# Kernel tuning notes

Hardware: AMD Instinct MI355X
Metric: run time of the kernel (lower is better)

## Reference

```python
import jax, jax.numpy as jnp
import numpy as np

HID, XD, ZD, K = 512, 128, 64, 3
B, T = 64, 1024

def setup_inputs() -> dict:
    key = jax.random.key(0)
    ks = jax.random.split(key, 10)
    s = lambda *d: 1.0 / np.sqrt(d[0])
    return {
        "x_seq": jax.random.normal(ks[0], (B, T, XD), jnp.float32),
        "conv_w": jax.random.normal(ks[1], (K, XD, HID), jnp.float32) * (1.0/np.sqrt(K*XD)),
        "conv_b": jnp.zeros((HID,), jnp.float32),
        "Wx": jax.random.normal(ks[2], (HID, 4*HID), jnp.float32) * (1.0/np.sqrt(HID)),
        "Wh": jax.random.normal(ks[3], (HID, 4*HID), jnp.float32) * (1.0/np.sqrt(HID)),
        "b": jnp.zeros((4*HID,), jnp.float32),
        "W1": jax.random.normal(ks[4], (HID, HID), jnp.float32) * (1.0/np.sqrt(HID)),
        "b1": jnp.zeros((HID,), jnp.float32),
        "W2": jax.random.normal(ks[5], (HID, 2*ZD), jnp.float32) * (1.0/np.sqrt(HID)),
        "b2": jnp.zeros((2*ZD,), jnp.float32),
    }

def _forward(x_seq, conv_w, conv_b, Wx, Wh, b, W1, b1, W2, b2):
    # Conv1D, SAME padding: (B, T, x_dim) -> (B, T, HID)
    conv = jax.lax.conv_general_dilated(
        x_seq, conv_w, window_strides=(1,), padding="SAME",
        dimension_numbers=("NWC", "WIO", "NWC")) + conv_b

    def step(carry, x_t):
        c, h = carry
        # flax LSTMCell: gates i,f,g,o; input dense (no bias) + hidden dense (bias)
        z = x_t @ Wx + h @ Wh + b  # (B, 4*HID)
        i, f, g, o = jnp.split(z, 4, axis=-1)
        i, f, o = jax.nn.sigmoid(i), jax.nn.sigmoid(f), jax.nn.sigmoid(o)
        g = jnp.tanh(g)
        c_new = f * c + i * g
        h_new = o * jnp.tanh(c_new)
        return (c_new, h_new), h_new

    c0 = jnp.zeros((conv.shape[0], HID), conv.dtype)
    h0 = jnp.zeros((conv.shape[0], HID), conv.dtype)
    _, h_seq = jax.lax.scan(step, (c0, h0), jnp.swapaxes(conv, 0, 1))  # (T, B, HID)
    h_seq = jnp.swapaxes(h_seq, 0, 1)  # (B, T, HID)

    # per-step 2-layer MLP head, applied vectorized over (B, T)
    x = jax.nn.relu(h_seq @ W1 + b1)
    out = x @ W2 + b2  # (B, T, 2*ZD)
    mu, log_sigma = jnp.split(out, 2, axis=-1)
    return mu, log_sigma

def reference(x_seq, conv_w, conv_b, Wx, Wh, b, W1, b1, W2, b2):
    return _forward(x_seq, conv_w, conv_b, Wx, Wh, b, W1, b1, W2, b2)
```

## Files before the change

### kernel.cpp

```cpp
#include <hip/hip_runtime.h>
#include <math.h>

typedef unsigned short u16;
typedef unsigned int   u32;
typedef unsigned long long u64;
typedef _Float16 f16;
typedef __attribute__((ext_vector_type(8))) _Float16 f16x8;
typedef __attribute__((ext_vector_type(4))) float    f32x4;

#define T_SEQ 1024
#define NB    64
#define HID   512
#define KC    384
#define G4    2048
#define MR    (NB*T_SEQ)
#define ZD2   128

__device__ __align__(16) f16   g_xwin[(size_t)MR*KC];
__device__ __align__(16) f16   g_cwxt[(size_t)G4*KC];
__device__              float  g_bb[G4];
__device__ __align__(16) f16   g_whT[(size_t)G4*HID];
__device__ __align__(16) f16   g_w1T[(size_t)HID*HID];
__device__ __align__(16) f16   g_w2T[(size_t)ZD2*HID];
__device__              float  g_b1f[HID];
__device__              float  g_b2f[ZD2];
__device__ __align__(16) float g_XW[(size_t)MR*G4];
__device__ __align__(16) f16   g_hseq[(size_t)MR*HID];
__device__ __align__(16) f16   g_tmp1[(size_t)MR*HID];
__device__ __align__(16) u64   g_hstep[(size_t)(T_SEQ+1)*NB*128];
__device__              int    g_flags[T_SEQ*64];
__device__              int    g_in_fp32;

__device__ inline float bf2f(u16 u){ union{u32 i; float f;} v; v.i = ((u32)u)<<16; return v.f; }
__device__ inline u16  f2bf(float f){ union{u32 i; float f;} v; v.f = f; u32 u = v.i;
                                      return (u16)((u + 0x7fffu + ((u>>16)&1u))>>16); }
__device__ inline float load_in(const void* p, size_t i){
  return g_in_fp32 ? ((const float*)p)[i] : bf2f(((const u16*)p)[i]);
}
__device__ inline float fsig(float x){
  return __builtin_amdgcn_rcpf(1.f + __builtin_amdgcn_exp2f(-1.44269504f*x));
}
__device__ inline float ftanh(float x){
  x = fminf(fmaxf(x, -10.f), 10.f);
  float e = __builtin_amdgcn_exp2f(2.88539008f*x);
  return (e - 1.f) * __builtin_amdgcn_rcpf(e + 1.f);
}

__global__ void k_probe(const void* x){
  __shared__ int cnt;
  if (threadIdx.x == 0) cnt = 0;
  __syncthreads();
  int loc = 0;
  for (int i = threadIdx.x; i < 4096; i += 256){
    float a = fabsf(bf2f(((const u16*)x)[i]));
    if (a > 0.01f && a < 10.f) loc++;
  }
  atomicAdd(&cnt, loc);
  __syncthreads();
  if (threadIdx.x == 0) g_in_fp32 = (cnt < 3276) ? 1 : 0;
}

__global__ void k_init(const void* b1, const void* b2){
  int i = blockIdx.x*256 + threadIdx.x;
  if (i < HID)        g_b1f[i] = load_in(b1, i);
  if (i < ZD2)        g_b2f[i] = load_in(b2, i);
  if (i < T_SEQ*64)   g_flags[i] = 0;
  if (i < NB*128)     g_hstep[i] = 0ULL;
}

__global__ void k_combine(const void* conv_w, const void* conv_b, const void* Wx, const void* b){
  int j  = blockIdx.x*256 + threadIdx.x;
  int kc = blockIdx.y;
  float acc = 0.f;
  if (kc < KC){
    for (int m = 0; m < HID; ++m)
      acc += load_in(conv_w, (size_t)kc*HID + m) * load_in(Wx, (size_t)m*G4 + j);
    g_cwxt[(size_t)j*KC + kc] = (f16)acc;
  } else {
    for (int m = 0; m < HID; ++m)
      acc += load_in(conv_b, m) * load_in(Wx, (size_t)m*G4 + j);
    g_bb[j] = acc + load_in(b, j);
  }
}

__device__ inline void trans_body(const void* src, f16* dst, int R, int C){
  size_t i = (size_t)blockIdx.x*256 + threadIdx.x;
  if (i >= (size_t)R*C) return;
  int c = (int)(i / (size_t)R), r = (int)(i % (size_t)R);
  dst[i] = (f16)load_in(src, (size_t)r*C + c);
}
__global__ void k_trans_wh(const void* Wh){ trans_body(Wh, g_whT, HID, G4); }
__global__ void k_trans_w1(const void* W1){ trans_body(W1, g_w1T, HID, HID); }
__global__ void k_trans_w2(const void* W2){ trans_body(W2, g_w2T, HID, ZD2); }

__global__ void k_xwin(const void* x){
  size_t i = (size_t)blockIdx.x*256 + threadIdx.x;
  if (i >= (size_t)MR*KC) return;
  int row = (int)(i / KC), kc = (int)(i % KC);
  int k = kc >> 7, c = kc & 127;
  int b = row >> 10, t = row & 1023;
  int ts = t - 1 + k;
  float v = 0.f;
  if (ts >= 0 && ts < T_SEQ) v = load_in(x, ((size_t)b*T_SEQ + ts)*128 + c);
  g_xwin[i] = (f16)v;
}

template<int MODE, int K>
__device__ inline void gemm_body(const f16* __restrict__ A, const f16* __restrict__ BT,
                                 const float* __restrict__ bias, void* __restrict__ C, int N){
  const int tid = threadIdx.x;
  const int w = tid >> 6, lane = tid & 63;
  const int q = lane >> 4, ln = lane & 15;
  const int n0 = blockIdx.x * 128;
  const int m0 = blockIdx.y * 64;
  const f16* ap = A + (size_t)(m0 + w*16 + ln)*K + q*8;
  const f16* bp = BT + (size_t)(n0 + ln)*K + q*8;
  f32x4 acc[8] = {};
  #pragma unroll 4
  for (int k = 0; k < K; k += 32){
    f16x8 af = *(const f16x8*)(ap + k);
    #pragma unroll
    for (int nt = 0; nt < 8; ++nt){
      f16x8 bf = *(const f16x8*)(bp + (size_t)nt*16*K + k);
      acc[nt] = __builtin_amdgcn_mfma_f32_16x16x32_f16(af, bf, acc[nt], 0, 0, 0);
    }
  }
  const int f32o = g_in_fp32;
  #pragma unroll
  for (int nt = 0; nt < 8; ++nt){
    const int col = n0 + nt*16 + ln;
    const float bv = bias[col];
    #pragma unroll
    for (int r = 0; r < 4; ++r){
      const int row = m0 + w*16 + q*4 + r;
      float v = acc[nt][r] + bv;
      if (MODE == 0){
        ((float*)C)[(size_t)row*N + col] = v;
      } else if (MODE == 1){
        ((f16*)C)[(size_t)row*N + col] = (f16)fmaxf(v, 0.f);
      } else {
        size_t idx = (col < 64) ? ((size_t)row*64 + col)
                                : (4194304UL + (size_t)row*64 + (size_t)(col - 64));
        if (f32o) ((float*)C)[idx] = v;
        else      ((u16*)C)[idx]   = f2bf(v);
      }
    }
  }
}
__global__ __launch_bounds__(256) void k_gemm_xw(){   gemm_body<0,KC >(g_xwin, g_cwxt, g_bb,  g_XW,   G4 ); }
__global__ __launch_bounds__(256) void k_gemm_mlp1(){ gemm_body<1,HID>(g_hseq, g_w1T,  g_b1f, g_tmp1, HID); }
__global__ __launch_bounds__(256) void k_gemm_mlp2(void* out){ gemm_body<2,HID>(g_tmp1, g_w2T, g_b2f, out, ZD2); }

__global__ __launch_bounds__(256) void k_lstm(){
  __shared__ __align__(16) f16 whs[32*520];
  const int g   = blockIdx.x;
  const int tid = threadIdx.x;
  const int w = tid >> 6, lane = tid & 63;
  const int q = lane >> 4, ln = lane & 15;

  for (int idx = tid; idx < 32*HID; idx += 256){
    int r = idx >> 9, k = idx & 511;
    int zcol = (r >> 3)*HID + g*8 + (r & 7);
    whs[r*520 + k] = g_whT[(size_t)zcol*HID + k];
  }
  __syncthreads();

  const int  c8 = ln & 7;
  const bool lo = ln < 8;
  const int  zc0  = (lo ? 0 : HID)       + g*8 + c8;
  const int  zc1  = (lo ? 2*HID : 3*HID) + g*8 + c8;
  const int  colh = g*8 + c8;
  const int  am   = w*16 + ln;
  float c_st[4] = {0.f, 0.f, 0.f, 0.f};

  for (int t = 0; t < T_SEQ; ++t){
    float xwa[4], xwb[4];
    #pragma unroll
    for (int r = 0; r < 4; ++r){
      size_t base = ((size_t)((w*16 + q*4 + r)*T_SEQ + t))*G4;
      xwa[r] = g_XW[base + zc0];
      xwb[r] = g_XW[base + zc1];
    }
    if (t > 0){
      if (tid < 64){
        while (__hip_atomic_load(&g_flags[(t-1)*64 + tid],
                                 __ATOMIC_RELAXED, __HIP_MEMORY_SCOPE_AGENT) == 0) {}
      }
      __syncthreads();
    }
    const u64* hrow = g_hstep + ((size_t)t*NB + am)*128 + q*2;
    u64 hv[32];
    #pragma unroll
    for (int kk = 0; kk < 16; ++kk){
      hv[2*kk]   = __hip_atomic_load(hrow + (size_t)kk*8,     __ATOMIC_RELAXED, __HIP_MEMORY_SCOPE_AGENT);
      hv[2*kk+1] = __hip_atomic_load(hrow + (size_t)kk*8 + 1, __ATOMIC_RELAXED, __HIP_MEMORY_SCOPE_AGENT);
    }
    f32x4 a0 = {0.f,0.f,0.f,0.f}, a1 = {0.f,0.f,0.f,0.f};
    #pragma unroll
    for (int kk = 0; kk < 16; ++kk){
      union { u64 u[2]; f16x8 v; } cvt;
      cvt.u[0] = hv[2*kk]; cvt.u[1] = hv[2*kk+1];
      f16x8 af = cvt.v;
      int k = kk*32;
      f16x8 b0 = *(const f16x8*)&whs[(0*16 + ln)*520 + k + q*8];
      f16x8 b1 = *(const f16x8*)&whs[(1*16 + ln)*520 + k + q*8];
      a0 = __builtin_amdgcn_mfma_f32_16x16x32_f16(af, b0, a0, 0, 0, 0);
      a1 = __builtin_amdgcn_mfma_f32_16x16x32_f16(af, b1, a1, 0, 0, 0);
    }
    f16 h16v[4];
    #pragma unroll
    for (int r = 0; r < 4; ++r){
      float z0 = a0[r] + xwa[r];
      float z1 = a1[r] + xwb[r];
      float zf = __shfl_xor(z0, 8, 64);
      float zo = __shfl_xor(z1, 8, 64);
      float iv = fsig(z0);
      float fv = fsig(zf);
      float gv = ftanh(z1);
      float ov = fsig(zo);
      float cn = fv*c_st[r] + iv*gv;
      c_st[r] = cn;
      float hvf = ov*ftanh(cn);
      f16 h16 = (f16)hvf;
      h16v[r] = h16;
      u32 me = (u32)__builtin_bit_cast(u16, h16);
      u32 p1 = me | (((u32)__shfl_xor((int)me, 1, 64)) << 16);
      u32 p2 = (u32)__shfl_xor((int)p1, 2, 64);
      u64 pk = (u64)p1 | ((u64)p2 << 32);
      if (lo && (c8 & 3) == 0){
        int m = w*16 + q*4 + r;
        __hip_atomic_store(g_hstep + ((size_t)(t+1)*NB + m)*128 + (size_t)g*2 + (c8>>2),
                           pk, __ATOMIC_RELAXED, __HIP_MEMORY_SCOPE_AGENT);
      }
    }
    asm volatile("s_waitcnt vmcnt(0)" ::: "memory");
    __syncthreads();
    if (tid == 0)
      __hip_atomic_store(&g_flags[t*64 + g], 1, __ATOMIC_RELAXED, __HIP_MEMORY_SCOPE_AGENT);
    if (lo){
      #pragma unroll
      for (int r = 0; r < 4; ++r){
        int m = w*16 + q*4 + r;
        g_hseq[((size_t)m*T_SEQ + t)*HID + colh] = h16v[r];
      }
    }
  }
}

extern "C" void kernel_launch(void* const* d_in, const int* in_sizes, int n_in,
                              void* d_out, int out_size, void* d_ws, size_t ws_size,
                              hipStream_t stream){
  const void* x      = d_in[0];
  const void* conv_w = d_in[1];
  const void* conv_b = d_in[2];
  const void* Wx     = d_in[3];
  const void* Wh     = d_in[4];
  const void* b      = d_in[5];
  const void* W1     = d_in[6];
  const void* b1     = d_in[7];
  const void* W2     = d_in[8];
  const void* b2     = d_in[9];
  (void)in_sizes; (void)n_in; (void)out_size; (void)d_ws; (void)ws_size;

  hipLaunchKernelGGL(k_probe,   dim3(1),        dim3(256), 0, stream, x);
  hipLaunchKernelGGL(k_init,    dim3(256),      dim3(256), 0, stream, b1, b2);
  hipLaunchKernelGGL(k_combine, dim3(8, 385),   dim3(256), 0, stream, conv_w, conv_b, Wx, b);
  hipLaunchKernelGGL(k_trans_wh,dim3(4096),     dim3(256), 0, stream, Wh);
  hipLaunchKernelGGL(k_trans_w1,dim3(1024),     dim3(256), 0, stream, W1);
  hipLaunchKernelGGL(k_trans_w2,dim3(256),      dim3(256), 0, stream, W2);
  hipLaunchKernelGGL(k_xwin,    dim3(98304),    dim3(256), 0, stream, x);
  hipLaunchKernelGGL(k_gemm_xw, dim3(16, 1024), dim3(256), 0, stream);
  hipLaunchKernelGGL(k_lstm,    dim3(64),       dim3(256), 0, stream);
  hipLaunchKernelGGL(k_gemm_mlp1, dim3(4, 1024), dim3(256), 0, stream);
  hipLaunchKernelGGL(k_gemm_mlp2, dim3(1, 1024), dim3(256), 0, stream, d_out);
}
```

Baseline: 7.831 ms.

## Replace LSTM step flags with sentinel-polled hidden state and register-resident weights

The persistent LSTM kernel drops the per-step flag array and block barrier. The hidden-state buffer is pre-filled with an all-ones sentinel, and each wave polls its own h slice with cache-bypassing vector loads until no sentinel remains. Wh slices now live in registers instead of LDS, the next step's XW values are prefetched, and MFMA accumulation is split into two chains for more instruction-level parallelism. The cost is an extra fill kernel over the whole hstep buffer, a risk if a real fp16 pair ever matches the sentinel pattern, and higher register pressure.

```diff
diff --git a/kernel.cpp b/kernel.cpp
--- a/kernel.cpp
+++ b/kernel.cpp
@@ -7,6 +7,7 @@
 typedef _Float16 f16;
 typedef __attribute__((ext_vector_type(8))) _Float16 f16x8;
 typedef __attribute__((ext_vector_type(4))) float    f32x4;
+typedef __attribute__((ext_vector_type(4))) u32      u32x4;
 
 #define T_SEQ 1024
 #define NB    64
@@ -28,7 +29,6 @@
 __device__ __align__(16) f16   g_hseq[(size_t)MR*HID];
 __device__ __align__(16) f16   g_tmp1[(size_t)MR*HID];
 __device__ __align__(16) u64   g_hstep[(size_t)(T_SEQ+1)*NB*128];
-__device__              int    g_flags[T_SEQ*64];
 __device__              int    g_in_fp32;
 
 __device__ inline float bf2f(u16 u){ union{u32 i; float f;} v; v.i = ((u32)u)<<16; return v.f; }
@@ -64,8 +64,14 @@
   int i = blockIdx.x*256 + threadIdx.x;
   if (i < HID)        g_b1f[i] = load_in(b1, i);
   if (i < ZD2)        g_b2f[i] = load_in(b2, i);
-  if (i < T_SEQ*64)   g_flags[i] = 0;
   if (i < NB*128)     g_hstep[i] = 0ULL;
+}
+
+__global__ void k_fill(){
+  size_t i = (size_t)blockIdx.x*256 + threadIdx.x;
+  u64* p = g_hstep + (size_t)NB*128;
+  const size_t n = (size_t)T_SEQ*NB*128;
+  for (size_t j = i; j < n; j += (size_t)4096*256) p[j] = ~0ULL;
 }
 
 __global__ void k_combine(const void* conv_w, const void* conv_b, const void* Wx, const void* b){
@@ -151,62 +157,104 @@
 __global__ __launch_bounds__(256) void k_gemm_mlp1(){ gemm_body<1,HID>(g_hseq, g_w1T,  g_b1f, g_tmp1, HID); }
 __global__ __launch_bounds__(256) void k_gemm_mlp2(void* out){ gemm_body<2,HID>(g_tmp1, g_w2T, g_b2f, out, ZD2); }
 
-__global__ __launch_bounds__(256) void k_lstm(){
-  __shared__ __align__(16) f16 whs[32*520];
+__global__ __launch_bounds__(256, 1) void k_lstm(){
   const int g   = blockIdx.x;
   const int tid = threadIdx.x;
   const int w = tid >> 6, lane = tid & 63;
   const int q = lane >> 4, ln = lane & 15;
-
-  for (int idx = tid; idx < 32*HID; idx += 256){
-    int r = idx >> 9, k = idx & 511;
-    int zcol = (r >> 3)*HID + g*8 + (r & 7);
-    whs[r*520 + k] = g_whT[(size_t)zcol*HID + k];
-  }
-  __syncthreads();
-
   const int  c8 = ln & 7;
   const bool lo = ln < 8;
   const int  zc0  = (lo ? 0 : HID)       + g*8 + c8;
   const int  zc1  = (lo ? 2*HID : 3*HID) + g*8 + c8;
   const int  colh = g*8 + c8;
   const int  am   = w*16 + ln;
+
+  const size_t zA = (size_t)((ln>>3)*HID     + g*8 + c8) * HID;
+  const size_t zB = (size_t)((2+(ln>>3))*HID + g*8 + c8) * HID;
+  f16x8 bf0[16], bf1[16];
+  #pragma unroll
+  for (int kk = 0; kk < 16; ++kk){
+    bf0[kk] = *(const f16x8*)&g_whT[zA + kk*32 + q*8];
+    bf1[kk] = *(const f16x8*)&g_whT[zB + kk*32 + q*8];
+  }
+
   float c_st[4] = {0.f, 0.f, 0.f, 0.f};
 
+  size_t rowb[4];
+  #pragma unroll
+  for (int r = 0; r < 4; ++r) rowb[r] = (size_t)(w*16 + q*4 + r)*T_SEQ*G4;
+  float xwa[4], xwb[4];
+  #pragma unroll
+  for (int r = 0; r < 4; ++r){
+    xwa[r] = g_XW[rowb[r] + zc0];
+    xwb[r] = g_XW[rowb[r] + zc1];
+  }
+
+  u64 addr = (u64)(const void*)(g_hstep + ((size_t)am)*128 + (size_t)q*2);
+
   for (int t = 0; t < T_SEQ; ++t){
-    float xwa[4], xwb[4];
+    u32x4 hr[16];
+    for (;;){
+      asm volatile(
+        "global_load_dwordx4 %0, %16, off sc0 sc1\n"
+        "global_load_dwordx4 %1, %16, off offset:64 sc0 sc1\n"
+        "global_load_dwordx4 %2, %16, off offset:128 sc0 sc1\n"
+        "global_load_dwordx4 %3, %16, off offset:192 sc0 sc1\n"
+        "global_load_dwordx4 %4, %16, off offset:256 sc0 sc1\n"
+        "global_load_dwordx4 %5, %16, off offset:320 sc0 sc1\n"
+        "global_load_dwordx4 %6, %16, off offset:384 sc0 sc1\n"
+        "global_load_dwordx4 %7, %16, off offset:448 sc0 sc1\n"
+        "global_load_dwordx4 %8, %16, off offset:512 sc0 sc1\n"
+        "global_load_dwordx4 %9, %16, off offset:576 sc0 sc1\n"
+        "global_load_dwordx4 %10, %16, off offset:640 sc0 sc1\n"
+        "global_load_dwordx4 %11, %16, off offset:704 sc0 sc1\n"
+        "global_load_dwordx4 %12, %16, off offset:768 sc0 sc1\n"
+        "global_load_dwordx4 %13, %16, off offset:832 sc0 sc1\n"
+        "global_load_dwordx4 %14, %16, off offset:896 sc0 sc1\n"
+        "global_load_dwordx4 %15, %16, off offset:960 sc0 sc1\n"
+        "s_waitcnt vmcnt(0)"
+        : "=&v"(hr[0]),  "=&v"(hr[1]),  "=&v"(hr[2]),  "=&v"(hr[3]),
+          "=&v"(hr[4]),  "=&v"(hr[5]),  "=&v"(hr[6]),  "=&v"(hr[7]),
+          "=&v"(hr[8]),  "=&v"(hr[9]),  "=&v"(hr[10]), "=&v"(hr[11]),
+          "=&v"(hr[12]), "=&v"(hr[13]), "=&v"(hr[14]), "=&v"(hr[15])
+        : "v"(addr)
+        : "memory");
+      u32 bad = 0;
+      #pragma unroll
+      for (int i = 0; i < 16; ++i){
+        bad |= (u32)((hr[i].x & hr[i].y) == 0xFFFFFFFFu);
+        bad |= (u32)((hr[i].z & hr[i].w) == 0xFFFFFFFFu);
+      }
+      if (!__any((int)bad)) break;
+      __builtin_amdgcn_s_sleep(1);
+    }
+    addr += (u64)NB*128*8;
+
+    const int tn = (t+1 < T_SEQ) ? (t+1) : t;
+    float xna[4], xnb[4];
     #pragma unroll
     for (int r = 0; r < 4; ++r){
-      size_t base = ((size_t)((w*16 + q*4 + r)*T_SEQ + t))*G4;
-      xwa[r] = g_XW[base + zc0];
-      xwb[r] = g_XW[base + zc1];
-    }
-    if (t > 0){
-      if (tid < 64){
-        while (__hip_atomic_load(&g_flags[(t-1)*64 + tid],
-                                 __ATOMIC_RELAXED, __HIP_MEMORY_SCOPE_AGENT) == 0) {}
-      }
-      __syncthreads();
-    }
-    const u64* hrow = g_hstep + ((size_t)t*NB + am)*128 + q*2;
-    u64 hv[32];
+      const size_t base = rowb[r] + (size_t)tn*G4;
+      xna[r] = g_XW[base + zc0];
+      xnb[r] = g_XW[base + zc1];
+    }
+
+    f32x4 a0a = {0.f,0.f,0.f,0.f}, a0b = {0.f,0.f,0.f,0.f};
+    f32x4 a1a = {0.f,0.f,0.f,0.f}, a1b = {0.f,0.f,0.f,0.f};
     #pragma unroll
     for (int kk = 0; kk < 16; ++kk){
-      hv[2*kk]   = __hip_atomic_load(hrow + (size_t)kk*8,     __ATOMIC_RELAXED, __HIP_MEMORY_SCOPE_AGENT);
-      hv[2*kk+1] = __hip_atomic_load(hrow + (size_t)kk*8 + 1, __ATOMIC_RELAXED, __HIP_MEMORY_SCOPE_AGENT);
-    }
-    f32x4 a0 = {0.f,0.f,0.f,0.f}, a1 = {0.f,0.f,0.f,0.f};
-    #pragma unroll
-    for (int kk = 0; kk < 16; ++kk){
-      union { u64 u[2]; f16x8 v; } cvt;
-      cvt.u[0] = hv[2*kk]; cvt.u[1] = hv[2*kk+1];
-      f16x8 af = cvt.v;
-      int k = kk*32;
-      f16x8 b0 = *(const f16x8*)&whs[(0*16 + ln)*520 + k + q*8];
-      f16x8 b1 = *(const f16x8*)&whs[(1*16 + ln)*520 + k + q*8];
-      a0 = __builtin_amdgcn_mfma_f32_16x16x32_f16(af, b0, a0, 0, 0, 0);
-      a1 = __builtin_amdgcn_mfma_f32_16x16x32_f16(af, b1, a1, 0, 0, 0);
-    }
+      f16x8 af = __builtin_bit_cast(f16x8, hr[kk]);
+      if (kk & 1){
+        a0b = __builtin_amdgcn_mfma_f32_16x16x32_f16(af, bf0[kk], a0b, 0, 0, 0);
+        a1b = __builtin_amdgcn_mfma_f32_16x16x32_f16(af, bf1[kk], a1b, 0, 0, 0);
+      } else {
+        a0a = __builtin_amdgcn_mfma_f32_16x16x32_f16(af, bf0[kk], a0a, 0, 0, 0);
+        a1a = __builtin_amdgcn_mfma_f32_16x16x32_f16(af, bf1[kk], a1a, 0, 0, 0);
+      }
+    }
+    f32x4 a0 = a0a + a0b;
+    f32x4 a1 = a1a + a1b;
+
     f16 h16v[4];
     #pragma unroll
     for (int r = 0; r < 4; ++r){
@@ -233,10 +281,6 @@
                            pk, __ATOMIC_RELAXED, __HIP_MEMORY_SCOPE_AGENT);
       }
     }
-    asm volatile("s_waitcnt vmcnt(0)" ::: "memory");
-    __syncthreads();
-    if (tid == 0)
-      __hip_atomic_store(&g_flags[t*64 + g], 1, __ATOMIC_RELAXED, __HIP_MEMORY_SCOPE_AGENT);
     if (lo){
       #pragma unroll
       for (int r = 0; r < 4; ++r){
@@ -244,6 +288,8 @@
         g_hseq[((size_t)m*T_SEQ + t)*HID + colh] = h16v[r];
       }
     }
+    #pragma unroll
+    for (int r = 0; r < 4; ++r){ xwa[r] = xna[r]; xwb[r] = xnb[r]; }
   }
 }
 
@@ -264,6 +310,7 @@
 
   hipLaunchKernelGGL(k_probe,   dim3(1),        dim3(256), 0, stream, x);
   hipLaunchKernelGGL(k_init,    dim3(256),      dim3(256), 0, stream, b1, b2);
+  hipLaunchKernelGGL(k_fill,    dim3(4096),     dim3(256), 0, stream);
   hipLaunchKernelGGL(k_combine, dim3(8, 385),   dim3(256), 0, stream, conv_w, conv_b, Wx, b);
   hipLaunchKernelGGL(k_trans_wh,dim3(4096),     dim3(256), 0, stream, Wh);
   hipLaunchKernelGGL(k_trans_w1,dim3(1024),     dim3(256), 0, stream, W1);
```

New measurement: 8.156 ms. 4.2% more time.

## Replace LSTM flag barrier with sentinel-polled hidden state and halve workgroups

Applied to the files above, without the earlier changes.

The recurrent LSTM kernel drops the per-step flag array and __syncthreads handshake. The hidden-state buffer is pre-filled with an all-ones sentinel, and each wave polls its own 16-byte slices with cache-bypassing loads until no sentinel remains. Each of 32 workgroups now computes 16 hidden columns across all four gates (4 MFMA tiles per wave, split accumulators, swizzled LDS), so the gate shuffles go away. The next step's input projection is prefetched during the wait. The risks are an extra fill kernel writing the whole step buffer, and correctness depending on the sentinel never occurring as a real packed fp16 pair (all-ones is a NaN pattern).

```diff
diff --git a/kernel.cpp b/kernel.cpp
--- a/kernel.cpp
+++ b/kernel.cpp
@@ -7,6 +7,7 @@
 typedef _Float16 f16;
 typedef __attribute__((ext_vector_type(8))) _Float16 f16x8;
 typedef __attribute__((ext_vector_type(4))) float    f32x4;
+typedef __attribute__((ext_vector_type(4))) u32      u32x4;
 
 #define T_SEQ 1024
 #define NB    64
@@ -15,6 +16,7 @@
 #define G4    2048
 #define MR    (NB*T_SEQ)
 #define ZD2   128
+#define NWG   32
 
 __device__ __align__(16) f16   g_xwin[(size_t)MR*KC];
 __device__ __align__(16) f16   g_cwxt[(size_t)G4*KC];
@@ -28,7 +30,6 @@
 __device__ __align__(16) f16   g_hseq[(size_t)MR*HID];
 __device__ __align__(16) f16   g_tmp1[(size_t)MR*HID];
 __device__ __align__(16) u64   g_hstep[(size_t)(T_SEQ+1)*NB*128];
-__device__              int    g_flags[T_SEQ*64];
 __device__              int    g_in_fp32;
 
 __device__ inline float bf2f(u16 u){ union{u32 i; float f;} v; v.i = ((u32)u)<<16; return v.f; }
@@ -44,6 +45,10 @@
   x = fminf(fmaxf(x, -10.f), 10.f);
   float e = __builtin_amdgcn_exp2f(2.88539008f*x);
   return (e - 1.f) * __builtin_amdgcn_rcpf(e + 1.f);
+}
+__device__ inline int slice_ok(u32x4 v){
+  return (v.x != 0xFFFFFFFFu) & (v.y != 0xFFFFFFFFu) &
+         (v.z != 0xFFFFFFFFu) & (v.w != 0xFFFFFFFFu);
 }
 
 __global__ void k_probe(const void* x){
@@ -64,8 +69,14 @@
   int i = blockIdx.x*256 + threadIdx.x;
   if (i < HID)        g_b1f[i] = load_in(b1, i);
   if (i < ZD2)        g_b2f[i] = load_in(b2, i);
-  if (i < T_SEQ*64)   g_flags[i] = 0;
   if (i < NB*128)     g_hstep[i] = 0ULL;
+}
+
+__global__ void k_fill(){
+  size_t i = (size_t)blockIdx.x*256 + threadIdx.x;
+  u64* p = g_hstep + (size_t)NB*128;
+  const size_t n = (size_t)T_SEQ*NB*128;
+  for (size_t j = i; j < n; j += (size_t)4096*256) p[j] = ~0ULL;
 }
 
 __global__ void k_combine(const void* conv_w, const void* conv_b, const void* Wx, const void* b){
@@ -151,72 +162,106 @@
 __global__ __launch_bounds__(256) void k_gemm_mlp1(){ gemm_body<1,HID>(g_hseq, g_w1T,  g_b1f, g_tmp1, HID); }
 __global__ __launch_bounds__(256) void k_gemm_mlp2(void* out){ gemm_body<2,HID>(g_tmp1, g_w2T, g_b2f, out, ZD2); }
 
-__global__ __launch_bounds__(256) void k_lstm(){
-  __shared__ __align__(16) f16 whs[32*520];
+__global__ __launch_bounds__(256, 1) void k_lstm(){
+  __shared__ __align__(16) f16 whs[64*512];
   const int g   = blockIdx.x;
   const int tid = threadIdx.x;
   const int w = tid >> 6, lane = tid & 63;
   const int q = lane >> 4, ln = lane & 15;
-
-  for (int idx = tid; idx < 32*HID; idx += 256){
-    int r = idx >> 9, k = idx & 511;
-    int zcol = (r >> 3)*HID + g*8 + (r & 7);
-    whs[r*520 + k] = g_whT[(size_t)zcol*HID + k];
+  const int jcol = g*16 + ln;
+  const int am   = w*16 + ln;
+
+  for (int idx = tid; idx < 64*64; idx += 256){
+    int n = idx >> 6, k8 = (idx & 63) * 8;
+    int zcol = (n >> 4)*HID + g*16 + (n & 15);
+    *(f16x8*)&whs[(n << 9) | (k8 ^ ((n & 7) << 3))] =
+        *(const f16x8*)&g_whT[(size_t)zcol*HID + k8];
   }
   __syncthreads();
 
-  const int  c8 = ln & 7;
-  const bool lo = ln < 8;
-  const int  zc0  = (lo ? 0 : HID)       + g*8 + c8;
-  const int  zc1  = (lo ? 2*HID : 3*HID) + g*8 + c8;
-  const int  colh = g*8 + c8;
-  const int  am   = w*16 + ln;
   float c_st[4] = {0.f, 0.f, 0.f, 0.f};
 
+  size_t rowb[4];
+  #pragma unroll
+  for (int r = 0; r < 4; ++r) rowb[r] = (size_t)(w*16 + q*4 + r)*T_SEQ*G4;
+  float xw[4][4];
+  #pragma unroll
+  for (int nt = 0; nt < 4; ++nt)
+    #pragma unroll
+    for (int r = 0; r < 4; ++r)
+      xw[nt][r] = g_XW[rowb[r] + nt*HID + jcol];
+
+  u64 addr = (u64)(const void*)(g_hstep + ((size_t)am)*128 + (size_t)q*2);
+
+  #pragma unroll 1
   for (int t = 0; t < T_SEQ; ++t){
-    float xwa[4], xwb[4];
+    u32x4 hr[16];
+#define ISSUE(KK, OFF)                                                         \
+    asm volatile("global_load_dwordx4 %0, %1, off offset:" OFF " sc0 sc1"      \
+                 : "=v"(hr[KK]) : "v"(addr) : "memory");
+    ISSUE(0,"0")   ISSUE(1,"64")   ISSUE(2,"128")  ISSUE(3,"192")
+    ISSUE(4,"256") ISSUE(5,"320")  ISSUE(6,"384")  ISSUE(7,"448")
+    ISSUE(8,"512") ISSUE(9,"576")  ISSUE(10,"640") ISSUE(11,"704")
+    ISSUE(12,"768")ISSUE(13,"832") ISSUE(14,"896") ISSUE(15,"960")
+
+    const int tn = (t+1 < T_SEQ) ? (t+1) : t;
+    float xn[4][4];
+    #pragma unroll
+    for (int nt = 0; nt < 4; ++nt)
+      #pragma unroll
+      for (int r = 0; r < 4; ++r)
+        xn[nt][r] = g_XW[rowb[r] + (size_t)tn*G4 + nt*HID + jcol];
+
+    u32 need = 0xFFFFu;
+    for (;;){
+      asm volatile("s_waitcnt vmcnt(0)"
+        : "+v"(hr[0]),  "+v"(hr[1]),  "+v"(hr[2]),  "+v"(hr[3]),
+          "+v"(hr[4]),  "+v"(hr[5]),  "+v"(hr[6]),  "+v"(hr[7]),
+          "+v"(hr[8]),  "+v"(hr[9]),  "+v"(hr[10]), "+v"(hr[11]),
+          "+v"(hr[12]), "+v"(hr[13]), "+v"(hr[14]), "+v"(hr[15])
+        :: "memory");
+      u32 nb = 0;
+      #pragma unroll
+      for (int kk = 0; kk < 16; ++kk)
+        if (need & (1u<<kk))
+          if (!__all(slice_ok(hr[kk]))) nb |= (1u<<kk);
+      if (!nb) break;
+      need = nb;
+#define REISSUE(KK, OFF)                                                       \
+      if (need & (1u<<KK))                                                     \
+        asm volatile("global_load_dwordx4 %0, %1, off offset:" OFF " sc0 sc1"  \
+                     : "=v"(hr[KK]) : "v"(addr) : "memory");
+      REISSUE(0,"0")   REISSUE(1,"64")   REISSUE(2,"128")  REISSUE(3,"192")
+      REISSUE(4,"256") REISSUE(5,"320")  REISSUE(6,"384")  REISSUE(7,"448")
+      REISSUE(8,"512") REISSUE(9,"576")  REISSUE(10,"640") REISSUE(11,"704")
+      REISSUE(12,"768")REISSUE(13,"832") REISSUE(14,"896") REISSUE(15,"960")
+#undef REISSUE
+    }
+#undef ISSUE
+
+    f32x4 aA[4] = {}, aB[4] = {};
+    #pragma unroll
+    for (int kk = 0; kk < 16; ++kk){
+      f16x8 af = __builtin_bit_cast(f16x8, hr[kk]);
+      #pragma unroll
+      for (int nt = 0; nt < 4; ++nt){
+        f16x8 bf = *(const f16x8*)&whs[((nt*16 + ln) << 9) |
+                                       ((kk*32 + q*8) ^ ((ln & 7) << 3))];
+        if (kk & 1) aB[nt] = __builtin_amdgcn_mfma_f32_16x16x32_f16(af, bf, aB[nt], 0, 0, 0);
+        else        aA[nt] = __builtin_amdgcn_mfma_f32_16x16x32_f16(af, bf, aA[nt], 0, 0, 0);
+      }
+    }
+
+    f16 h16v[4];
     #pragma unroll
     for (int r = 0; r < 4; ++r){
-      size_t base = ((size_t)((w*16 + q*4 + r)*T_SEQ + t))*G4;
-      xwa[r] = g_XW[base + zc0];
-      xwb[r] = g_XW[base + zc1];
-    }
-    if (t > 0){
-      if (tid < 64){
-        while (__hip_atomic_load(&g_flags[(t-1)*64 + tid],
-                                 __ATOMIC_RELAXED, __HIP_MEMORY_SCOPE_AGENT) == 0) {}
-      }
-      __syncthreads();
-    }
-    const u64* hrow = g_hstep + ((size_t)t*NB + am)*128 + q*2;
-    u64 hv[32];
-    #pragma unroll
-    for (int kk = 0; kk < 16; ++kk){
-      hv[2*kk]   = __hip_atomic_load(hrow + (size_t)kk*8,     __ATOMIC_RELAXED, __HIP_MEMORY_SCOPE_AGENT);
-      hv[2*kk+1] = __hip_atomic_load(hrow + (size_t)kk*8 + 1, __ATOMIC_RELAXED, __HIP_MEMORY_SCOPE_AGENT);
-    }
-    f32x4 a0 = {0.f,0.f,0.f,0.f}, a1 = {0.f,0.f,0.f,0.f};
-    #pragma unroll
-    for (int kk = 0; kk < 16; ++kk){
-      union { u64 u[2]; f16x8 v; } cvt;
-      cvt.u[0] = hv[2*kk]; cvt.u[1] = hv[2*kk+1];
-      f16x8 af = cvt.v;
-      int k = kk*32;
-      f16x8 b0 = *(const f16x8*)&whs[(0*16 + ln)*520 + k + q*8];
-      f16x8 b1 = *(const f16x8*)&whs[(1*16 + ln)*520 + k + q*8];
-      a0 = __builtin_amdgcn_mfma_f32_16x16x32_f16(af, b0, a0, 0, 0, 0);
-      a1 = __builtin_amdgcn_mfma_f32_16x16x32_f16(af, b1, a1, 0, 0, 0);
-    }
-    f16 h16v[4];
-    #pragma unroll
-    for (int r = 0; r < 4; ++r){
-      float z0 = a0[r] + xwa[r];
-      float z1 = a1[r] + xwb[r];
-      float zf = __shfl_xor(z0, 8, 64);
-      float zo = __shfl_xor(z1, 8, 64);
-      float iv = fsig(z0);
+      float zi = aA[0][r] + aB[0][r] + xw[0][r];
+      float zf = aA[1][r] + aB[1][r] + xw[1][r];
+      float zg = aA[2][r] + aB[2][r] + xw[2][r];
+      float zo = aA[3][r] + aB[3][r] + xw[3][r];
+      float iv = fsig(zi);
       float fv = fsig(zf);
-      float gv = ftanh(z1);
+      float gv = ftanh(zg);
       float ov = fsig(zo);
       float cn = fv*c_st[r] + iv*gv;
       c_st[r] = cn;
@@ -224,26 +269,24 @@
       f16 h16 = (f16)hvf;
       h16v[r] = h16;
       u32 me = (u32)__builtin_bit_cast(u16, h16);
-      u32 p1 = me | (((u32)__shfl_xor((int)me, 1, 64)) << 16);
-      u32 p2 = (u32)__shfl_xor((int)p1, 2, 64);
-      u64 pk = (u64)p1 | ((u64)p2 << 32);
-      if (lo && (c8 & 3) == 0){
+      u32 p  = me | (((u32)__shfl_xor((int)me, 1, 64)) << 16);
+      if ((ln & 1) == 0){
         int m = w*16 + q*4 + r;
-        __hip_atomic_store(g_hstep + ((size_t)(t+1)*NB + m)*128 + (size_t)g*2 + (c8>>2),
-                           pk, __ATOMIC_RELAXED, __HIP_MEMORY_SCOPE_AGENT);
+        __hip_atomic_store((u32*)g_hstep + ((size_t)(t+1)*NB + m)*256 + (jcol >> 1),
+                           p, __ATOMIC_RELAXED, __HIP_MEMORY_SCOPE_AGENT);
       }
     }
-    asm volatile("s_waitcnt vmcnt(0)" ::: "memory");
-    __syncthreads();
-    if (tid == 0)
-      __hip_atomic_store(&g_flags[t*64 + g], 1, __ATOMIC_RELAXED, __HIP_MEMORY_SCOPE_AGENT);
-    if (lo){
+    #pragma unroll
+    for (int r = 0; r < 4; ++r){
+      int m = w*16 + q*4 + r;
+      g_hseq[((size_t)m*T_SEQ + t)*HID + jcol] = h16v[r];
+    }
+    #pragma unroll
+    for (int nt = 0; nt < 4; ++nt)
       #pragma unroll
-      for (int r = 0; r < 4; ++r){
-        int m = w*16 + q*4 + r;
-        g_hseq[((size_t)m*T_SEQ + t)*HID + colh] = h16v[r];
-      }
-    }
+      for (int r = 0; r < 4; ++r)
+        xw[nt][r] = xn[nt][r];
+    addr += (u64)NB*128*8;
   }
 }
 
@@ -264,13 +307,14 @@
 
   hipLaunchKernelGGL(k_probe,   dim3(1),        dim3(256), 0, stream, x);
   hipLaunchKernelGGL(k_init,    dim3(256),      dim3(256), 0, stream, b1, b2);
+  hipLaunchKernelGGL(k_fill,    dim3(4096),     dim3(256), 0, stream);
   hipLaunchKernelGGL(k_combine, dim3(8, 385),   dim3(256), 0, stream, conv_w, conv_b, Wx, b);
   hipLaunchKernelGGL(k_trans_wh,dim3(4096),     dim3(256), 0, stream, Wh);
   hipLaunchKernelGGL(k_trans_w1,dim3(1024),     dim3(256), 0, stream, W1);
   hipLaunchKernelGGL(k_trans_w2,dim3(256),      dim3(256), 0, stream, W2);
   hipLaunchKernelGGL(k_xwin,    dim3(98304),    dim3(256), 0, stream, x);
   hipLaunchKernelGGL(k_gemm_xw, dim3(16, 1024), dim3(256), 0, stream);
-  hipLaunchKernelGGL(k_lstm,    dim3(64),       dim3(256), 0, stream);
+  hipLaunchKernelGGL(k_lstm,    dim3(NWG),      dim3(256), 0, stream);
   hipLaunchKernelGGL(k_gemm_mlp1, dim3(4, 1024), dim3(256), 0, stream);
   hipLaunchKernelGGL(k_gemm_mlp2, dim3(1, 1024), dim3(256), 0, stream, d_out);
 }
```

Result: slower. 9.013 ms (+15.1%).
